# Optimization experiments

Measured on AMD Instinct MI355X. Metric: run time of the kernel, lower is better.

Reference implementation:

```python
import jax, jax.numpy as jnp
import numpy as np
from jax import lax

DEPTH = 3  # signature truncation depth
B, L, I, H, O = 256, 512, 32, 16, 10
SIG_DIM = H + H**2 + H**3  # 4368 = signatory.signature_channels(16, 3)


def setup_inputs() -> dict:
    key = jax.random.key(0)
    ks = jax.random.split(key, 7)
    s = 1.0 / np.sqrt(H).astype(np.float32)
    sf = 1.0 / np.sqrt(SIG_DIM).astype(np.float32)
    return {
        "X": jax.random.normal(ks[0], (B, L, I), jnp.float32),
        "W_ih": jax.random.uniform(ks[1], (4 * H, I), jnp.float32, -s, s),
        "W_hh": jax.random.uniform(ks[2], (4 * H, H), jnp.float32, -s, s),
        "b_ih": jax.random.uniform(ks[3], (4 * H,), jnp.float32, -s, s),
        "b_hh": jax.random.uniform(ks[4], (4 * H,), jnp.float32, -s, s),
        "fc_w": jax.random.uniform(ks[5], (O, SIG_DIM), jnp.float32, -sf, sf),
        "fc_b": jax.random.uniform(ks[6], (O,), jnp.float32, -sf, sf),
    }


def _lstm(X, W_ih, W_hh, b_ih, b_hh):
    # torch nn.LSTM, single layer, batch_first, gate order (i, f, g, o)
    b, l, _ = X.shape
    h0 = jnp.zeros((b, H), X.dtype)
    c0 = jnp.zeros((b, H), X.dtype)
    # precompute input projection for all timesteps: [L, B, 4H]
    xw = jnp.swapaxes(jnp.einsum('bli,gi->blg', X, W_ih) + b_ih + b_hh, 0, 1)

    def step(carry, xw_t):
        h, c = carry
        gates = xw_t + h @ W_hh.T
        i, f, g, o = jnp.split(gates, 4, axis=-1)
        c = jax.nn.sigmoid(f) * c + jax.nn.sigmoid(i) * jnp.tanh(g)
        h = jax.nn.sigmoid(o) * jnp.tanh(c)
        return (h, c), h

    _, hs = lax.scan(step, (h0, c0), xw)  # hs: [L, B, H]
    return jnp.swapaxes(hs, 0, 1)  # [B, L, H]


def _outer(a, b):
    # batched flattened tensor product: [B, m] x [B, n] -> [B, m*n]
    return (a[:, :, None] * b[:, None, :]).reshape(a.shape[0], -1)


def _signature(h, depth):
    # signatory.signature: Chen's identity scan over path increments,
    # returns concatenated levels 1..depth: [B, C + C^2 + ... + C^depth]
    b, l, c = h.shape
    dx = jnp.swapaxes(h[:, 1:] - h[:, :-1], 0, 1)  # [L-1, B, C]
    S0 = tuple(jnp.zeros((b, c ** (k + 1)), h.dtype) for k in range(depth))

    def step(S, d):
        # exp(d) levels: e_k = d^{tensor k} / k!
        e = [d]
        for k in range(2, depth + 1):
            e.append(_outer(e[-1], d) / k)
        # S <- S (x) exp(d), truncated:  newS_k = S_k + sum_{j=1..k-1} S_{k-j} (x) e_j + e_k
        newS = []
        for k in range(1, depth + 1):
            acc = S[k - 1] + e[k - 1]
            for j in range(1, k):
                acc = acc + _outer(S[k - j - 1], e[j - 1])
            newS.append(acc)
        return tuple(newS), None

    S, _ = lax.scan(step, S0, dx)
    return jnp.concatenate(S, axis=-1)  # [B, SIG_DIM]


def reference(X, W_ih, W_hh, b_ih, b_hh, fc_w, fc_b):
    hseq = _lstm(X, W_ih, W_hh, b_ih, b_hh)           # [B, L, H]
    sig = _signature(hseq, DEPTH)                      # [B, SIG_DIM]
    out = sig @ fc_w.T + fc_b                          # [B, O]
    return out.reshape(-1, O)
```

## Files before the change

### kernel.cpp

```cpp
#include <hip/hip_runtime.h>

#define NB 256
#define NL 512
#define NI 32
#define NH 16
#define NG 64
#define SIGD 4368
#define XS 516

__device__ __forceinline__ float RL(float v, int lane) {
  return __builtin_bit_cast(float, __builtin_amdgcn_readlane(__builtin_bit_cast(int, v), lane));
}
template<int CTRL>
__device__ __forceinline__ float QB(float v) {
  return __builtin_bit_cast(float, __builtin_amdgcn_update_dpp(
      0, __builtin_bit_cast(int, v), CTRL, 0xF, 0xF, true));
}
__device__ __forceinline__ int segc(int k) {
  switch (k) {
    case 1: return 76;  case 2: return 148; case 3: return 220; case 4: return 292;
    case 5: return 364; case 6: return 436; case 7: return 504; case 8: return 511;
    default: return 0;
  }
}

__global__ __launch_bounds__(512, 1) void k_main(const float* __restrict__ X,
    const float* __restrict__ Wih, const float* __restrict__ bih,
    const float* __restrict__ bhh, const float* __restrict__ Whh,
    const float* __restrict__ fcw, const float* __restrict__ fcb,
    float* __restrict__ out) {
  __shared__ __align__(16) float xwT[NG * XS];
  __shared__ __align__(16) float slot[4352];
  __shared__ __align__(16) float red[80];
  __shared__ int prog;
  __shared__ int want;
  __shared__ int have;
  int tid = threadIdx.x;
  int wv = tid >> 6;
  int ln = tid & 63;
  int b = blockIdx.x;

  if (tid == 0) { prog = -1; want = 0; have = 0; }

  {
    const float Kg = (ln >= 32 && ln < 48) ? 2.885390082f : -1.442695041f;
    float w2[NI];
#pragma unroll
    for (int i = 0; i < 8; ++i) {
      float4 v = *(const float4*)(Wih + ln * NI + 4 * i);
      w2[4*i+0] = v.x; w2[4*i+1] = v.y; w2[4*i+2] = v.z; w2[4*i+3] = v.w;
    }
    float bias = bih[ln] + bhh[ln];
    const float* xb = X + (size_t)b * NL * NI;
#pragma unroll 4
    for (int t = 64 * wv; t < 64 * (wv + 1); ++t) {
      const float4* xr = (const float4*)(xb + t * NI);
      float x0 = bias, x1 = 0.f, x2 = 0.f, x3 = 0.f;
#pragma unroll
      for (int i = 0; i < 8; ++i) {
        float4 xv = xr[i];
        x0 += xv.x * w2[4*i+0]; x1 += xv.y * w2[4*i+1];
        x2 += xv.z * w2[4*i+2]; x3 += xv.w * w2[4*i+3];
      }
      xwT[ln * XS + t] = Kg * ((x0 + x1) + (x2 + x3));
    }
  }
  __syncthreads();

  if (wv == 0) {
    __asm__ __volatile__("s_setprio 3");
    const int q = ln & 3;
    const int j = ln >> 2;
    const int gmem = q * 16 + j;
    const bool isg = (q == 2);
    const float Kg = isg ? 2.885390082f : -1.442695041f;
    const float CT = 2.885390082f;
    const float Av = isg ? -2.0f : (q == 0 ? CT : 1.0f);
    const float Bv = isg ? 1.0f : 0.0f;
    float w[NH];
#pragma unroll
    for (int qq = 0; qq < 4; ++qq) {
      float4 v = *(const float4*)(Whh + gmem * NH + 4 * qq);
      w[4*qq+0] = Kg*v.x; w[4*qq+1] = Kg*v.y; w[4*qq+2] = Kg*v.z; w[4*qq+3] = Kg*v.w;
    }
    const float* xt = xwT + gmem * XS;
    float* hdst = xwT + j * XS + 4 * q;
    float4 xq[4];
#pragma unroll
    for (int i = 0; i < 4; ++i) xq[i] = *(const float4*)(xt + 4 * i);
    float cs = 0.0f, hval = 0.0f;
    float hst[4] = {0.f, 0.f, 0.f, 0.f};
    for (int tb = 0; tb < NL; tb += 16) {
#pragma unroll
      for (int k = 0; k < 16; ++k) {
        int t = tb + k;
        float hs[16];
#pragma unroll
        for (int u = 0; u < 16; ++u) hs[u] = RL(hval, 4 * u);
        float xval = ((const float*)xq)[k];
        if ((k & 3) == 3 && t + 16 < NL)
          xq[k >> 2] = *(const float4*)(xt + (t + 13));
        float a0 = xval, a1 = 0.f, a2 = 0.f, a3 = 0.f;
#pragma unroll
        for (int u = 0; u < 4; ++u) {
          a0 += hs[4*u+0] * w[4*u+0];
          a1 += hs[4*u+1] * w[4*u+1];
          a2 += hs[4*u+2] * w[4*u+2];
          a3 += hs[4*u+3] * w[4*u+3];
        }
        float acc = (a0 + a1) + (a2 + a3);
        float e = __builtin_amdgcn_exp2f(acc);
        float r = __builtin_amdgcn_rcpf(1.0f + e);
        float val = __builtin_fmaf(Av, r, Bv);
        float iv = QB<0x00>(val);
        float fv = QB<0x55>(val);
        float gv = QB<0xAA>(val);
        float ov = QB<0xFF>(val);
        cs = __builtin_fmaf(fv, cs, iv * gv);
        float e2 = __builtin_amdgcn_exp2f(cs);
        float tc = __builtin_fmaf(-2.0f, __builtin_amdgcn_rcpf(1.0f + e2), 1.0f);
        hval = ov * tc;
        hst[k & 3] = (q == (k >> 2)) ? hval : hst[k & 3];
      }
      float4 hv;
      hv.x = hst[0]; hv.y = hst[1]; hv.z = hst[2]; hv.w = hst[3];
      *(float4*)(hdst + tb) = hv;
      __asm__ __volatile__("" ::: "memory");
      if (ln == 0) *(volatile int*)&prog = tb + 15;
    }
    __asm__ __volatile__("s_setprio 0");
  }

  int seg;
  if (wv >= 1 && wv <= 6) seg = wv;
  else if (wv == 7) seg = 0;
  else seg = 7;
  const int ts = segc(seg);
  const int te = segc(seg + 1);
  const int bi = ln & 15;
  const int hi = ln >> 4;

  float s3[4][16];
  float s2[4] = {0.f, 0.f, 0.f, 0.f};
#pragma unroll
  for (int m = 0; m < 4; ++m)
#pragma unroll
    for (int cc = 0; cc < 16; ++cc) s3[m][cc] = 0.f;

  int avail;
  while ((avail = *(volatile int*)&prog) < ts) __builtin_amdgcn_s_sleep(2);
  __asm__ __volatile__("" ::: "memory");

  float hA[16], hB[16];
  float hAb, hBb;
  float hAa[4], hBa[4], h0a[4];
#pragma unroll
  for (int cc = 0; cc < 16; ++cc) hA[cc] = xwT[cc * XS + ts];
  hAb = xwT[bi * XS + ts];
#pragma unroll
  for (int m = 0; m < 4; ++m) { hAa[m] = xwT[(4 * m + hi) * XS + ts]; h0a[m] = hAa[m]; }

  auto SSTEP = [&](float (&hc16)[16], float& hcb, float (&hca)[4],
                   float (&hn16)[16], float& hnb, float (&hna)[4], int tn) {
#pragma unroll
    for (int cc = 0; cc < 16; ++cc) hn16[cc] = xwT[cc * XS + tn];
    hnb = xwT[bi * XS + tn];
    float d[16];
#pragma unroll
    for (int cc = 0; cc < 16; ++cc) d[cc] = hn16[cc] - hc16[cc];
    float db = hnb - hcb;
    float P[4];
#pragma unroll
    for (int m = 0; m < 4; ++m) {
      hna[m] = xwT[(4 * m + hi) * XS + tn];
      float da = hna[m] - hca[m];
      float s1 = hca[m] - h0a[m];
      P[m] = s2[m] + db * (0.5f * s1 + 0.166666666667f * da);
      s2[m] += db * (s1 + 0.5f * da);
    }
#pragma unroll
    for (int m = 0; m < 4; ++m)
#pragma unroll
      for (int cc = 0; cc < 16; ++cc)
        s3[m][cc] += P[m] * d[cc];
  };

  {
    int t = ts;
    for (; t + 2 <= te; t += 2) {
      int tn2 = t + 2;
      if (tn2 > avail) {
        while ((avail = *(volatile int*)&prog) < tn2) __builtin_amdgcn_s_sleep(2);
        __asm__ __volatile__("" ::: "memory");
      }
      SSTEP(hA, hAb, hAa, hB, hBb, hBa, t + 1);
      SSTEP(hB, hBb, hBa, hA, hAb, hAa, t + 2);
    }
    if (t < te) {
      if (te > avail) {
        while ((avail = *(volatile int*)&prog) < te) __builtin_amdgcn_s_sleep(2);
        __asm__ __volatile__("" ::: "memory");
      }
      SSTEP(hA, hAb, hAa, hB, hBb, hBa, t + 1);
    }
  }

  if (seg >= 1) {
    while (*(volatile int*)&want != seg) __builtin_amdgcn_s_sleep(8);
    __asm__ __volatile__("" ::: "memory");
#pragma unroll
    for (int m = 0; m < 4; ++m) slot[64 * m + ln] = s2[m];
#pragma unroll
    for (int m = 0; m < 4; ++m)
#pragma unroll
      for (int cc = 0; cc < 16; ++cc)
        slot[256 + 64 * ln + ((m * 16 + cc) ^ (ln & 31))] = s3[m][cc];
    __asm__ __volatile__("s_waitcnt lgkmcnt(0)" ::: "memory");
    if (ln == 0) *(volatile int*)&have = seg;
  } else {
    for (int k = 1; k <= 7; ++k) {
      if (ln == 0) *(volatile int*)&want = k;
      while (*(volatile int*)&have != k) __builtin_amdgcn_s_sleep(8);
      __asm__ __volatile__("" ::: "memory");
      const int ae_ = segc(k), be_ = segc(k + 1);
      float s1b[16];
#pragma unroll
      for (int cc = 0; cc < 16; ++cc)
        s1b[cc] = xwT[cc * XS + be_] - xwT[cc * XS + ae_];
      float s1bb = xwT[bi * XS + be_] - xwT[bi * XS + ae_];
      float s1aa[4];
#pragma unroll
      for (int m = 0; m < 4; ++m) {
        int a = 4 * m + hi;
        s1aa[m] = xwT[a * XS + ae_] - xwT[a * XS + 0];
      }
      float row[16];
#pragma unroll
      for (int cc = 0; cc < 16; ++cc) row[cc] = slot[bi * 16 + cc];
#pragma unroll
      for (int m = 0; m < 4; ++m) {
        float s2bo = slot[64 * m + ln];
#pragma unroll
        for (int cc = 0; cc < 16; ++cc)
          s3[m][cc] += slot[256 + 64 * ln + ((m * 16 + cc) ^ (ln & 31))]
                     + s2[m] * s1b[cc] + s1aa[m] * row[cc];
        s2[m] += s2bo + s1aa[m] * s1bb;
      }
    }
    float* sigb = xwT + 16 * XS;
    if (ln < 16) sigb[ln] = xwT[ln * XS + 511] - xwT[ln * XS + 0];
#pragma unroll
    for (int m = 0; m < 4; ++m) sigb[16 + 64 * m + ln] = s2[m];
#pragma unroll
    for (int m = 0; m < 4; ++m) {
#pragma unroll
      for (int qq = 0; qq < 4; ++qq) {
        float4 v;
        v.x = s3[m][4*qq+0]; v.y = s3[m][4*qq+1]; v.z = s3[m][4*qq+2]; v.w = s3[m][4*qq+3];
        *(float4*)(sigb + 272 + 1024 * m + 256 * hi + 16 * bi + 4 * qq) = v;
      }
    }
  }
  __syncthreads();

  {
    const float* sigb = xwT + 16 * XS;
    float acc[10];
#pragma unroll
    for (int o = 0; o < 10; ++o) acc[o] = 0.f;
    for (int k = tid; k < SIGD; k += 512) {
      float s = sigb[k];
#pragma unroll
      for (int o = 0; o < 10; ++o) acc[o] += s * fcw[o * SIGD + k];
    }
#pragma unroll
    for (int o = 0; o < 10; ++o) {
      float v = acc[o];
#pragma unroll
      for (int off = 32; off > 0; off >>= 1) v += __shfl_down(v, off);
      if (ln == 0) red[wv * 10 + o] = v;
    }
    __syncthreads();
    if (tid < 10) {
      float s = fcb[tid];
#pragma unroll
      for (int w = 0; w < 8; ++w) s += red[w * 10 + tid];
      out[b * 10 + tid] = s;
    }
  }
}

extern "C" void kernel_launch(void* const* d_in, const int* in_sizes, int n_in,
                              void* d_out, int out_size, void* d_ws, size_t ws_size,
                              hipStream_t stream) {
  const float* X   = (const float*)d_in[0];
  const float* Wih = (const float*)d_in[1];
  const float* Whh = (const float*)d_in[2];
  const float* bih = (const float*)d_in[3];
  const float* bhh = (const float*)d_in[4];
  const float* fcw = (const float*)d_in[5];
  const float* fcb = (const float*)d_in[6];
  float* out = (float*)d_out;
  k_main<<<NB, 512, 0, stream>>>(X, Wih, bih, bhh, Whh, fcw, fcb, out);
}
```

Measured before the change: 187.5 us.

## Process two batch rows per block with interleaved LSTM recurrences

Each block now handles two sequences. The recurrent wave interleaves two independent LSTM chains so their latency-bound dependency chains overlap, and the grid drops to 128 blocks. The input projection moves from LDS to a global workspace buffer to make room for two hidden-state buffers, two slot areas and two signature buffers. Each sequence's signature is split across fewer waves (4 and 3) with separate handshakes. This trades more per-wave signature work and global-memory xw reads for halving the serial recurrence count per CU.

After: 345.9 us. +84.5%, slower.

```diff
diff --git a/kernel.cpp b/kernel.cpp
--- a/kernel.cpp
+++ b/kernel.cpp
@@ -1,12 +1,12 @@
 #include <hip/hip_runtime.h>
 
-#define NB 256
+#define NB 128
 #define NL 512
 #define NI 32
 #define NH 16
 #define NG 64
 #define SIGD 4368
-#define XS 516
+#define HS 516
 
 __device__ __forceinline__ float RL(float v, int lane) {
   return __builtin_bit_cast(float, __builtin_amdgcn_readlane(__builtin_bit_cast(int, v), lane));
@@ -16,31 +16,26 @@
   return __builtin_bit_cast(float, __builtin_amdgcn_update_dpp(
       0, __builtin_bit_cast(int, v), CTRL, 0xF, 0xF, true));
 }
-__device__ __forceinline__ int segc(int k) {
-  switch (k) {
-    case 1: return 76;  case 2: return 148; case 3: return 220; case 4: return 292;
-    case 5: return 364; case 6: return 436; case 7: return 504; case 8: return 511;
-    default: return 0;
-  }
-}
 
 __global__ __launch_bounds__(512, 1) void k_main(const float* __restrict__ X,
     const float* __restrict__ Wih, const float* __restrict__ bih,
     const float* __restrict__ bhh, const float* __restrict__ Whh,
     const float* __restrict__ fcw, const float* __restrict__ fcb,
-    float* __restrict__ out) {
-  __shared__ __align__(16) float xwT[NG * XS];
-  __shared__ __align__(16) float slot[4352];
-  __shared__ __align__(16) float red[80];
-  __shared__ int prog;
-  __shared__ int want;
-  __shared__ int have;
+    float* __restrict__ out, float* __restrict__ xws) {
+  __shared__ __align__(16) float hA[NH * HS];
+  __shared__ __align__(16) float hB[NH * HS];
+  __shared__ __align__(16) float slotA[4352];
+  __shared__ __align__(16) float slotB[4352];
+  __shared__ __align__(16) float sigA[SIGD];
+  __shared__ __align__(16) float sigB[SIGD];
+  __shared__ float red[80];
+  __shared__ int prog, wantA, haveA, wantB, haveB;
   int tid = threadIdx.x;
   int wv = tid >> 6;
   int ln = tid & 63;
   int b = blockIdx.x;
 
-  if (tid == 0) { prog = -1; want = 0; have = 0; }
+  if (tid == 0) { prog = -1; wantA = 0; haveA = 0; wantB = 0; haveB = 0; }
 
   {
     const float Kg = (ln >= 32 && ln < 48) ? 2.885390082f : -1.442695041f;
@@ -51,18 +46,27 @@
       w2[4*i+0] = v.x; w2[4*i+1] = v.y; w2[4*i+2] = v.z; w2[4*i+3] = v.w;
     }
     float bias = bih[ln] + bhh[ln];
-    const float* xb = X + (size_t)b * NL * NI;
-#pragma unroll 4
-    for (int t = 64 * wv; t < 64 * (wv + 1); ++t) {
-      const float4* xr = (const float4*)(xb + t * NI);
-      float x0 = bias, x1 = 0.f, x2 = 0.f, x3 = 0.f;
-#pragma unroll
-      for (int i = 0; i < 8; ++i) {
-        float4 xv = xr[i];
-        x0 += xv.x * w2[4*i+0]; x1 += xv.y * w2[4*i+1];
-        x2 += xv.z * w2[4*i+2]; x3 += xv.w * w2[4*i+3];
-      }
-      xwT[ln * XS + t] = Kg * ((x0 + x1) + (x2 + x3));
+#pragma unroll
+    for (int bb = 0; bb < 2; ++bb) {
+      const float* xb = X + (size_t)(2 * b + bb) * NL * NI;
+      float* xg = xws + (size_t)b * (2 * NG * NL) + bb * NG * NL + ln * NL;
+      for (int t0 = 64 * wv; t0 < 64 * (wv + 1); t0 += 4) {
+        float o4[4];
+#pragma unroll
+        for (int s = 0; s < 4; ++s) {
+          const float4* xr = (const float4*)(xb + (t0 + s) * NI);
+          float x0 = bias, x1 = 0.f, x2 = 0.f, x3 = 0.f;
+#pragma unroll
+          for (int i = 0; i < 8; ++i) {
+            float4 xv = xr[i];
+            x0 += xv.x * w2[4*i+0]; x1 += xv.y * w2[4*i+1];
+            x2 += xv.z * w2[4*i+2]; x3 += xv.w * w2[4*i+3];
+          }
+          o4[s] = Kg * ((x0 + x1) + (x2 + x3));
+        }
+        float4 v; v.x = o4[0]; v.y = o4[1]; v.z = o4[2]; v.w = o4[3];
+        *(float4*)(xg + t0) = v;
+      }
     }
   }
   __syncthreads();
@@ -83,193 +87,245 @@
       float4 v = *(const float4*)(Whh + gmem * NH + 4 * qq);
       w[4*qq+0] = Kg*v.x; w[4*qq+1] = Kg*v.y; w[4*qq+2] = Kg*v.z; w[4*qq+3] = Kg*v.w;
     }
-    const float* xt = xwT + gmem * XS;
-    float* hdst = xwT + j * XS + 4 * q;
-    float4 xq[4];
-#pragma unroll
-    for (int i = 0; i < 4; ++i) xq[i] = *(const float4*)(xt + 4 * i);
-    float cs = 0.0f, hval = 0.0f;
-    float hst[4] = {0.f, 0.f, 0.f, 0.f};
+    const float* xta = xws + (size_t)b * (2 * NG * NL) + gmem * NL;
+    const float* xtb = xta + NG * NL;
+    float* hdA = hA + j * HS + 4 * q;
+    float* hdB = hB + j * HS + 4 * q;
+    float4 xqA[4], xqB[4];
+#pragma unroll
+    for (int i = 0; i < 4; ++i) { xqA[i] = *(const float4*)(xta + 4 * i);
+                                  xqB[i] = *(const float4*)(xtb + 4 * i); }
+    float csA = 0.f, hvA = 0.f, csB = 0.f, hvB = 0.f;
+    float hstA[4] = {0.f,0.f,0.f,0.f}, hstB[4] = {0.f,0.f,0.f,0.f};
     for (int tb = 0; tb < NL; tb += 16) {
 #pragma unroll
       for (int k = 0; k < 16; ++k) {
         int t = tb + k;
-        float hs[16];
-#pragma unroll
-        for (int u = 0; u < 16; ++u) hs[u] = RL(hval, 4 * u);
-        float xval = ((const float*)xq)[k];
-        if ((k & 3) == 3 && t + 16 < NL)
-          xq[k >> 2] = *(const float4*)(xt + (t + 13));
-        float a0 = xval, a1 = 0.f, a2 = 0.f, a3 = 0.f;
+        float hsA[16], hsB[16];
+#pragma unroll
+        for (int u = 0; u < 16; ++u) hsA[u] = RL(hvA, 4 * u);
+#pragma unroll
+        for (int u = 0; u < 16; ++u) hsB[u] = RL(hvB, 4 * u);
+        float xvA = ((const float*)xqA)[k];
+        float xvB = ((const float*)xqB)[k];
+        if ((k & 3) == 3 && t + 16 < NL) {
+          xqA[k >> 2] = *(const float4*)(xta + (t + 13));
+          xqB[k >> 2] = *(const float4*)(xtb + (t + 13));
+        }
+        float aA0 = xvA, aA1 = 0.f, aA2 = 0.f, aA3 = 0.f;
+        float aB0 = xvB, aB1 = 0.f, aB2 = 0.f, aB3 = 0.f;
 #pragma unroll
         for (int u = 0; u < 4; ++u) {
-          a0 += hs[4*u+0] * w[4*u+0];
-          a1 += hs[4*u+1] * w[4*u+1];
-          a2 += hs[4*u+2] * w[4*u+2];
-          a3 += hs[4*u+3] * w[4*u+3];
-        }
-        float acc = (a0 + a1) + (a2 + a3);
-        float e = __builtin_amdgcn_exp2f(acc);
-        float r = __builtin_amdgcn_rcpf(1.0f + e);
-        float val = __builtin_fmaf(Av, r, Bv);
-        float iv = QB<0x00>(val);
-        float fv = QB<0x55>(val);
-        float gv = QB<0xAA>(val);
-        float ov = QB<0xFF>(val);
-        cs = __builtin_fmaf(fv, cs, iv * gv);
-        float e2 = __builtin_amdgcn_exp2f(cs);
-        float tc = __builtin_fmaf(-2.0f, __builtin_amdgcn_rcpf(1.0f + e2), 1.0f);
-        hval = ov * tc;
-        hst[k & 3] = (q == (k >> 2)) ? hval : hst[k & 3];
-      }
-      float4 hv;
-      hv.x = hst[0]; hv.y = hst[1]; hv.z = hst[2]; hv.w = hst[3];
-      *(float4*)(hdst + tb) = hv;
+          aA0 += hsA[4*u+0] * w[4*u+0]; aB0 += hsB[4*u+0] * w[4*u+0];
+          aA1 += hsA[4*u+1] * w[4*u+1]; aB1 += hsB[4*u+1] * w[4*u+1];
+          aA2 += hsA[4*u+2] * w[4*u+2]; aB2 += hsB[4*u+2] * w[4*u+2];
+          aA3 += hsA[4*u+3] * w[4*u+3]; aB3 += hsB[4*u+3] * w[4*u+3];
+        }
+        float accA = (aA0 + aA1) + (aA2 + aA3);
+        float accB = (aB0 + aB1) + (aB2 + aB3);
+        float eA = __builtin_amdgcn_exp2f(accA);
+        float eB = __builtin_amdgcn_exp2f(accB);
+        float rA = __builtin_amdgcn_rcpf(1.0f + eA);
+        float rB = __builtin_amdgcn_rcpf(1.0f + eB);
+        float valA = __builtin_fmaf(Av, rA, Bv);
+        float valB = __builtin_fmaf(Av, rB, Bv);
+        float ivA = QB<0x00>(valA), ivB = QB<0x00>(valB);
+        float fvA = QB<0x55>(valA), fvB = QB<0x55>(valB);
+        float gvA = QB<0xAA>(valA), gvB = QB<0xAA>(valB);
+        float ovA = QB<0xFF>(valA), ovB = QB<0xFF>(valB);
+        csA = __builtin_fmaf(fvA, csA, ivA * gvA);
+        csB = __builtin_fmaf(fvB, csB, ivB * gvB);
+        float e2A = __builtin_amdgcn_exp2f(csA);
+        float e2B = __builtin_amdgcn_exp2f(csB);
+        float tcA = __builtin_fmaf(-2.0f, __builtin_amdgcn_rcpf(1.0f + e2A), 1.0f);
+        float tcB = __builtin_fmaf(-2.0f, __builtin_amdgcn_rcpf(1.0f + e2B), 1.0f);
+        hvA = ovA * tcA;
+        hvB = ovB * tcB;
+        hstA[k & 3] = (q == (k >> 2)) ? hvA : hstA[k & 3];
+        hstB[k & 3] = (q == (k >> 2)) ? hvB : hstB[k & 3];
+      }
+      float4 hva4; hva4.x = hstA[0]; hva4.y = hstA[1]; hva4.z = hstA[2]; hva4.w = hstA[3];
+      float4 hvb4; hvb4.x = hstB[0]; hvb4.y = hstB[1]; hvb4.z = hstB[2]; hvb4.w = hstB[3];
+      *(float4*)(hdA + tb) = hva4;
+      *(float4*)(hdB + tb) = hvb4;
       __asm__ __volatile__("" ::: "memory");
       if (ln == 0) *(volatile int*)&prog = tb + 15;
     }
     __asm__ __volatile__("s_setprio 0");
-  }
-
-  int seg;
-  if (wv >= 1 && wv <= 6) seg = wv;
-  else if (wv == 7) seg = 0;
-  else seg = 7;
-  const int ts = segc(seg);
-  const int te = segc(seg + 1);
-  const int bi = ln & 15;
-  const int hi = ln >> 4;
-
-  float s3[4][16];
-  float s2[4] = {0.f, 0.f, 0.f, 0.f};
-#pragma unroll
-  for (int m = 0; m < 4; ++m)
-#pragma unroll
-    for (int cc = 0; cc < 16; ++cc) s3[m][cc] = 0.f;
-
-  int avail;
-  while ((avail = *(volatile int*)&prog) < ts) __builtin_amdgcn_s_sleep(2);
-  __asm__ __volatile__("" ::: "memory");
-
-  float hA[16], hB[16];
-  float hAb, hBb;
-  float hAa[4], hBa[4], h0a[4];
-#pragma unroll
-  for (int cc = 0; cc < 16; ++cc) hA[cc] = xwT[cc * XS + ts];
-  hAb = xwT[bi * XS + ts];
-#pragma unroll
-  for (int m = 0; m < 4; ++m) { hAa[m] = xwT[(4 * m + hi) * XS + ts]; h0a[m] = hAa[m]; }
-
-  auto SSTEP = [&](float (&hc16)[16], float& hcb, float (&hca)[4],
-                   float (&hn16)[16], float& hnb, float (&hna)[4], int tn) {
-#pragma unroll
-    for (int cc = 0; cc < 16; ++cc) hn16[cc] = xwT[cc * XS + tn];
-    hnb = xwT[bi * XS + tn];
-    float d[16];
-#pragma unroll
-    for (int cc = 0; cc < 16; ++cc) d[cc] = hn16[cc] - hc16[cc];
-    float db = hnb - hcb;
-    float P[4];
-#pragma unroll
-    for (int m = 0; m < 4; ++m) {
-      hna[m] = xwT[(4 * m + hi) * XS + tn];
-      float da = hna[m] - hca[m];
-      float s1 = hca[m] - h0a[m];
-      P[m] = s2[m] + db * (0.5f * s1 + 0.166666666667f * da);
-      s2[m] += db * (s1 + 0.5f * da);
-    }
+  } else {
+    const float* hb; float* sb;
+    volatile int* wantp; volatile int* havep;
+    int sidx, ts, te;
+    if (wv == 1 || wv == 2 || wv == 3 || wv == 7) {
+      hb = hA; sb = slotA; wantp = &wantA; havep = &haveA;
+    } else {
+      hb = hB; sb = slotB; wantp = &wantB; havep = &haveB;
+    }
+    switch (wv) {
+      case 7: sidx = 0; ts = 0;   te = 160; break;
+      case 1: sidx = 1; ts = 160; te = 300; break;
+      case 2: sidx = 2; ts = 300; te = 420; break;
+      case 3: sidx = 3; ts = 420; te = 511; break;
+      case 6: sidx = 0; ts = 0;   te = 200; break;
+      case 4: sidx = 1; ts = 200; te = 380; break;
+      default: sidx = 2; ts = 380; te = 511; break;
+    }
+    const int bi = ln & 15;
+    const int hi = ln >> 4;
+
+    float s3[4][16];
+    float s2[4] = {0.f, 0.f, 0.f, 0.f};
 #pragma unroll
     for (int m = 0; m < 4; ++m)
 #pragma unroll
+      for (int cc = 0; cc < 16; ++cc) s3[m][cc] = 0.f;
+
+    int avail;
+    while ((avail = *(volatile int*)&prog) < ts) __builtin_amdgcn_s_sleep(2);
+    __asm__ __volatile__("" ::: "memory");
+
+    float hc16A[16], hc16B[16];
+    float hAb, hBb;
+    float hAa[4], hBa[4], h0a[4];
+#pragma unroll
+    for (int cc = 0; cc < 16; ++cc) hc16A[cc] = hb[cc * HS + ts];
+    hAb = hb[bi * HS + ts];
+#pragma unroll
+    for (int m = 0; m < 4; ++m) { hAa[m] = hb[(4 * m + hi) * HS + ts]; h0a[m] = hAa[m]; }
+
+    auto SSTEP = [&](float (&hc16)[16], float& hcb, float (&hca)[4],
+                     float (&hn16)[16], float& hnb, float (&hna)[4], int tn) {
+#pragma unroll
+      for (int cc = 0; cc < 16; ++cc) hn16[cc] = hb[cc * HS + tn];
+      hnb = hb[bi * HS + tn];
+      float d[16];
+#pragma unroll
+      for (int cc = 0; cc < 16; ++cc) d[cc] = hn16[cc] - hc16[cc];
+      float db = hnb - hcb;
+      float P[4];
+#pragma unroll
+      for (int m = 0; m < 4; ++m) {
+        hna[m] = hb[(4 * m + hi) * HS + tn];
+        float da = hna[m] - hca[m];
+        float s1 = hca[m] - h0a[m];
+        P[m] = s2[m] + db * (0.5f * s1 + 0.166666666667f * da);
+        s2[m] += db * (s1 + 0.5f * da);
+      }
+#pragma unroll
+      for (int m = 0; m < 4; ++m)
+#pragma unroll
+        for (int cc = 0; cc < 16; ++cc)
+          s3[m][cc] += P[m] * d[cc];
+    };
+
+    {
+      int t = ts;
+      for (; t + 2 <= te; t += 2) {
+        int tn2 = t + 2;
+        if (tn2 > avail) {
+          while ((avail = *(volatile int*)&prog) < tn2) __builtin_amdgcn_s_sleep(2);
+          __asm__ __volatile__("" ::: "memory");
+        }
+        SSTEP(hc16A, hAb, hAa, hc16B, hBb, hBa, t + 1);
+        SSTEP(hc16B, hBb, hBa, hc16A, hAb, hAa, t + 2);
+      }
+      if (t < te) {
+        if (te > avail) {
+          while ((avail = *(volatile int*)&prog) < te) __builtin_amdgcn_s_sleep(2);
+          __asm__ __volatile__("" ::: "memory");
+        }
+        SSTEP(hc16A, hAb, hAa, hc16B, hBb, hBa, t + 1);
+      }
+    }
+
+    auto COMB = [&](const float* hb2, const float* sb2, int ae_, int be_) {
+      float s1b[16];
+#pragma unroll
       for (int cc = 0; cc < 16; ++cc)
-        s3[m][cc] += P[m] * d[cc];
-  };
-
-  {
-    int t = ts;
-    for (; t + 2 <= te; t += 2) {
-      int tn2 = t + 2;
-      if (tn2 > avail) {
-        while ((avail = *(volatile int*)&prog) < tn2) __builtin_amdgcn_s_sleep(2);
-        __asm__ __volatile__("" ::: "memory");
-      }
-      SSTEP(hA, hAb, hAa, hB, hBb, hBa, t + 1);
-      SSTEP(hB, hBb, hBa, hA, hAb, hAa, t + 2);
-    }
-    if (t < te) {
-      if (te > avail) {
-        while ((avail = *(volatile int*)&prog) < te) __builtin_amdgcn_s_sleep(2);
-        __asm__ __volatile__("" ::: "memory");
-      }
-      SSTEP(hA, hAb, hAa, hB, hBb, hBa, t + 1);
-    }
-  }
-
-  if (seg >= 1) {
-    while (*(volatile int*)&want != seg) __builtin_amdgcn_s_sleep(8);
-    __asm__ __volatile__("" ::: "memory");
-#pragma unroll
-    for (int m = 0; m < 4; ++m) slot[64 * m + ln] = s2[m];
-#pragma unroll
-    for (int m = 0; m < 4; ++m)
-#pragma unroll
-      for (int cc = 0; cc < 16; ++cc)
-        slot[256 + 64 * ln + ((m * 16 + cc) ^ (ln & 31))] = s3[m][cc];
-    __asm__ __volatile__("s_waitcnt lgkmcnt(0)" ::: "memory");
-    if (ln == 0) *(volatile int*)&have = seg;
-  } else {
-    for (int k = 1; k <= 7; ++k) {
-      if (ln == 0) *(volatile int*)&want = k;
-      while (*(volatile int*)&have != k) __builtin_amdgcn_s_sleep(8);
-      __asm__ __volatile__("" ::: "memory");
-      const int ae_ = segc(k), be_ = segc(k + 1);
-      float s1b[16];
-#pragma unroll
-      for (int cc = 0; cc < 16; ++cc)
-        s1b[cc] = xwT[cc * XS + be_] - xwT[cc * XS + ae_];
-      float s1bb = xwT[bi * XS + be_] - xwT[bi * XS + ae_];
+        s1b[cc] = hb2[cc * HS + be_] - hb2[cc * HS + ae_];
+      float s1bb = hb2[bi * HS + be_] - hb2[bi * HS + ae_];
       float s1aa[4];
 #pragma unroll
       for (int m = 0; m < 4; ++m) {
         int a = 4 * m + hi;
-        s1aa[m] = xwT[a * XS + ae_] - xwT[a * XS + 0];
+        s1aa[m] = hb2[a * HS + ae_] - hb2[a * HS + 0];
       }
       float row[16];
 #pragma unroll
-      for (int cc = 0; cc < 16; ++cc) row[cc] = slot[bi * 16 + cc];
+      for (int cc = 0; cc < 16; ++cc) row[cc] = sb2[bi * 16 + cc];
 #pragma unroll
       for (int m = 0; m < 4; ++m) {
-        float s2bo = slot[64 * m + ln];
+        float s2bo = sb2[64 * m + ln];
 #pragma unroll
         for (int cc = 0; cc < 16; ++cc)
-          s3[m][cc] += slot[256 + 64 * ln + ((m * 16 + cc) ^ (ln & 31))]
+          s3[m][cc] += sb2[256 + 64 * ln + ((m * 16 + cc) ^ (ln & 31))]
                      + s2[m] * s1b[cc] + s1aa[m] * row[cc];
         s2[m] += s2bo + s1aa[m] * s1bb;
       }
-    }
-    float* sigb = xwT + 16 * XS;
-    if (ln < 16) sigb[ln] = xwT[ln * XS + 511] - xwT[ln * XS + 0];
-#pragma unroll
-    for (int m = 0; m < 4; ++m) sigb[16 + 64 * m + ln] = s2[m];
-#pragma unroll
-    for (int m = 0; m < 4; ++m) {
-#pragma unroll
-      for (int qq = 0; qq < 4; ++qq) {
-        float4 v;
-        v.x = s3[m][4*qq+0]; v.y = s3[m][4*qq+1]; v.z = s3[m][4*qq+2]; v.w = s3[m][4*qq+3];
-        *(float4*)(sigb + 272 + 1024 * m + 256 * hi + 16 * bi + 4 * qq) = v;
-      }
+    };
+    auto EMIT = [&](float* sg, const float* hb2) {
+      if (ln < 16) sg[ln] = hb2[ln * HS + 511] - hb2[ln * HS + 0];
+#pragma unroll
+      for (int m = 0; m < 4; ++m) sg[16 + 64 * m + ln] = s2[m];
+#pragma unroll
+      for (int m = 0; m < 4; ++m) {
+#pragma unroll
+        for (int qq = 0; qq < 4; ++qq) {
+          float4 v;
+          v.x = s3[m][4*qq+0]; v.y = s3[m][4*qq+1]; v.z = s3[m][4*qq+2]; v.w = s3[m][4*qq+3];
+          *(float4*)(sg + 272 + 1024 * m + 256 * hi + 16 * bi + 4 * qq) = v;
+        }
+      }
+    };
+
+    if (wv == 7) {
+      if (ln == 0) *(volatile int*)&wantA = 1;
+      while (*(volatile int*)&haveA != 1) __builtin_amdgcn_s_sleep(8);
+      __asm__ __volatile__("" ::: "memory");
+      COMB(hA, slotA, 160, 300);
+      if (ln == 0) *(volatile int*)&wantA = 2;
+      while (*(volatile int*)&haveA != 2) __builtin_amdgcn_s_sleep(8);
+      __asm__ __volatile__("" ::: "memory");
+      COMB(hA, slotA, 300, 420);
+      if (ln == 0) *(volatile int*)&wantA = 3;
+      while (*(volatile int*)&haveA != 3) __builtin_amdgcn_s_sleep(8);
+      __asm__ __volatile__("" ::: "memory");
+      COMB(hA, slotA, 420, 511);
+      EMIT(sigA, hA);
+    } else if (wv == 6) {
+      if (ln == 0) *(volatile int*)&wantB = 1;
+      while (*(volatile int*)&haveB != 1) __builtin_amdgcn_s_sleep(8);
+      __asm__ __volatile__("" ::: "memory");
+      COMB(hB, slotB, 200, 380);
+      if (ln == 0) *(volatile int*)&wantB = 2;
+      while (*(volatile int*)&haveB != 2) __builtin_amdgcn_s_sleep(8);
+      __asm__ __volatile__("" ::: "memory");
+      COMB(hB, slotB, 380, 511);
+      EMIT(sigB, hB);
+    } else {
+      while (*(volatile int*)wantp != sidx) __builtin_amdgcn_s_sleep(8);
+      __asm__ __volatile__("" ::: "memory");
+#pragma unroll
+      for (int m = 0; m < 4; ++m) sb[64 * m + ln] = s2[m];
+#pragma unroll
+      for (int m = 0; m < 4; ++m)
+#pragma unroll
+        for (int cc = 0; cc < 16; ++cc)
+          sb[256 + 64 * ln + ((m * 16 + cc) ^ (ln & 31))] = s3[m][cc];
+      __asm__ __volatile__("s_waitcnt lgkmcnt(0)" ::: "memory");
+      if (ln == 0) *(volatile int*)havep = sidx;
     }
   }
   __syncthreads();
 
   {
-    const float* sigb = xwT + 16 * XS;
+    const float* sg = (wv < 4) ? sigA : sigB;
+    const int wb = wv & 3;
     float acc[10];
 #pragma unroll
     for (int o = 0; o < 10; ++o) acc[o] = 0.f;
-    for (int k = tid; k < SIGD; k += 512) {
-      float s = sigb[k];
+    for (int k = wb * 64 + ln; k < SIGD; k += 256) {
+      float s = sg[k];
 #pragma unroll
       for (int o = 0; o < 10; ++o) acc[o] += s * fcw[o * SIGD + k];
     }
@@ -284,8 +340,14 @@
     if (tid < 10) {
       float s = fcb[tid];
 #pragma unroll
-      for (int w = 0; w < 8; ++w) s += red[w * 10 + tid];
-      out[b * 10 + tid] = s;
+      for (int w8 = 0; w8 < 4; ++w8) s += red[w8 * 10 + tid];
+      out[(2 * b) * 10 + tid] = s;
+    } else if (tid >= 64 && tid < 74) {
+      int o = tid - 64;
+      float s = fcb[o];
+#pragma unroll
+      for (int w8 = 4; w8 < 8; ++w8) s += red[w8 * 10 + o];
+      out[(2 * b + 1) * 10 + o] = s;
     }
   }
 }
@@ -301,5 +363,5 @@
   const float* fcw = (const float*)d_in[5];
   const float* fcb = (const float*)d_in[6];
   float* out = (float*)d_out;
-  k_main<<<NB, 512, 0, stream>>>(X, Wih, bih, bhh, Whh, fcw, fcb, out);
+  k_main<<<NB, 512, 0, stream>>>(X, Wih, bih, bhh, Whh, fcw, fcb, out, (float*)d_ws);
 }
```
